# Kernel tuning notes

Hardware: AMD Instinct MI355X
Metric: run time of the kernel (lower is better)

Reference implementation:

```python
import jax, jax.numpy as jnp
import numpy as np

B, N, DIM, H, DH, PDIM, ED = 2, 384, 256, 4, 64, 128, 16
EPS = 1e-8


def _ln(x, g, b):
    m = x.mean(-1, keepdims=True)
    v = ((x - m) ** 2).mean(-1, keepdims=True)
    return (x - m) / jnp.sqrt(v + 1e-5) * g + b


def setup_inputs() -> dict:
    key = jax.random.key(0)
    ks = iter(jax.random.split(key, 48))
    def rn(shape, s=0.02):
        return jax.random.normal(next(ks), shape, jnp.float32) * s
    z = lambda *s: jnp.zeros(s, jnp.float32)
    o = lambda *s: jnp.ones(s, jnp.float32)
    return dict(
        feats=jax.random.normal(next(ks), (B, N, DIM), jnp.float32),
        coors=jax.random.normal(next(ks), (B, N, 3), jnp.float32),
        edges=jax.random.normal(next(ks), (B, N, N, ED), jnp.float32),
        gamma=o(DIM),
        w_qkv=rn((DIM, 3 * H * DH)),
        w_gate=z(DIM, 2 * H), b_gate=jnp.full((2 * H,), 10.0, jnp.float32),
        w_th=rn((H, H), 0.3),
        w_e1=rn((H + ED, 2 * (H + ED))), w_e2=rn((2 * (H + ED), H)),
        w_c=rn((H, H)),
        w_cg=rn((H, H)), b_cg=z(H),
        coors_scale=o(1),
        coors_combine=jax.random.normal(next(ks), (H,), jnp.float32),
        pb_w0=rn((1, PDIM)), pb_b0=z(PDIM), pb_g0=o(PDIM), pb_be0=z(PDIM),
        pb_w1=rn((PDIM, PDIM)), pb_b1=z(PDIM), pb_g1=o(PDIM), pb_be1=z(PDIM),
        pb_w2=rn((PDIM, PDIM)), pb_b2=z(PDIM), pb_g2=o(PDIM), pb_be2=z(PDIM),
        w_qkpos=rn((PDIM, H)), b_qkpos=z(H),
        w_vpos=rn((PDIM, H * DH)), b_vpos=z(H * DH),
        w_out=rn((H * DH, DIM)), b_out=z(DIM),
    )


def reference(feats, coors, edges, gamma, w_qkv, w_gate, b_gate, w_th, w_e1, w_e2,
              w_c, w_cg, b_cg, coors_scale, coors_combine,
              pb_w0, pb_b0, pb_g0, pb_be0, pb_w1, pb_b1, pb_g1, pb_be1,
              pb_w2, pb_b2, pb_g2, pb_be2, w_qkpos, b_qkpos, w_vpos, b_vpos,
              w_out, b_out):
    b, n, _ = feats.shape
    h, dh = H, DH
    x = _ln(feats, gamma, 0.0)                                  # pre-norm (beta is a zero buffer)
    rel_coors = coors[:, :, None, :] - coors[:, None, :, :]      # b i j 3
    rel_dist = jnp.linalg.norm(rel_coors, axis=-1)               # b i j

    qkv = x @ w_qkv
    q, k, v = jnp.split(qkv, 3, axis=-1)
    q = q.reshape(b, n, h, dh).transpose(0, 2, 1, 3)             # b h n d
    k = k.reshape(b, n, h, dh).transpose(0, 2, 1, 3)
    v = v.reshape(b, n, h, dh).transpose(0, 2, 1, 3)

    gates = jax.nn.sigmoid(x @ w_gate + b_gate).reshape(b, n, 2, h)
    out_gate = gates[:, :, 0].transpose(0, 2, 1)[..., None]      # b h n 1
    rel_out_gate = gates[:, :, 1].transpose(0, 2, 1)[..., None]  # b h n 1

    # dynamic position bias MLP on pairwise distances (input_dim=1)
    p = rel_dist[..., None]                                      # b i j 1
    p = jax.nn.silu(_ln(p @ pb_w0 + pb_b0, pb_g0, pb_be0))
    p = jax.nn.silu(_ln(p @ pb_w1 + pb_b1, pb_g1, pb_be1))
    p = jax.nn.silu(_ln(p @ pb_w2 + pb_b2, pb_g2, pb_be2))       # b i j pdim
    qk_pos = (p @ w_qkpos + b_qkpos).transpose(0, 3, 1, 2)       # b h i j
    value_pos = (p @ w_vpos + b_vpos).reshape(b, n, n, h, dh).transpose(0, 3, 1, 2, 4)  # b h i j d

    q = q * (dh ** -0.5)
    qk = jnp.einsum('bhid,bhjd->bhij', q, k) + qk_pos            # b h i j

    # edge MLP fused with per-head scores
    qk_e = jnp.concatenate([qk.transpose(0, 2, 3, 1), edges], axis=-1)  # b i j (h+ed)
    cmi = jax.nn.gelu(qk_e @ w_e1, approximate=False) @ w_e2     # b i j h
    qk = cmi.transpose(0, 3, 1, 2)                               # b h i j

    # coordinate attention branch (edge variant: GELU -> Linear(h,h))
    coor_weights = jax.nn.gelu(cmi, approximate=False) @ w_c     # b i j h
    coor_attn = jax.nn.softmax(coor_weights, axis=-2)            # softmax over j
    rel_sign = cmi @ w_cg + b_cg                                 # b i j h

    nrm = jnp.linalg.norm(rel_coors, axis=-1, keepdims=True)
    rel_norm = rel_coors / jnp.maximum(nrm, EPS) * coors_scale   # CoorsNorm, b i j 3

    attn = jax.nn.softmax(qk, axis=-1)
    attn = jnp.einsum('hg,bgij->bhij', w_th, attn)               # talking heads 1x1 conv

    node_out = jnp.einsum('bhij,bhjd->bhid', attn, v) \
             + jnp.einsum('bhij,bhijd->bhid', attn, value_pos)   # b h i d

    w = coor_attn * rel_sign                                     # b i j h
    coors_out = jnp.einsum('bijh,bijc->bhic', w, rel_norm)       # b h i 3

    node_out = node_out * out_gate
    coors_out = coors_out * rel_out_gate
    coors_out = jnp.einsum('bhic,h->bic', coors_out, coors_combine)
    node_out = node_out.transpose(0, 2, 1, 3).reshape(b, n, h * dh)
    return node_out @ w_out + b_out, coors_out
```

## Files before the change

kernel.cpp:

```cpp
#include <hip/hip_runtime.h>
#include <hip/hip_bf16.h>

#define B_   2
#define N_   384
#define DIM_ 256
#define H_   4
#define DH_  64
#define PD_  128
#define ED_  16
#define NU2_ ((B_ * N_ * N_) / 16)

typedef _Float16 v8h __attribute__((ext_vector_type(8)));
typedef float    v4f __attribute__((ext_vector_type(4)));

__device__ __forceinline__ float rcp_(float x) { return __builtin_amdgcn_rcpf(x); }

__device__ __forceinline__ float erf_fast(float x) {
    float ax = fabsf(x);
    float t = rcp_(fmaf(0.3275911f, ax, 1.0f));
    float y = t * fmaf(t, fmaf(t, fmaf(t, fmaf(t, 1.061405429f, -1.453152027f),
                                       1.421413741f), -0.284496736f), 0.254829592f);
    float r = 1.0f - y * __expf(-ax * ax);
    return (x < 0.f) ? -r : r;
}
__device__ __forceinline__ float gelu_(float x) {
    return 0.5f * x * (1.0f + erf_fast(x * 0.70710678118654752f));
}
__device__ __forceinline__ float silu_(float x) {
    return x * rcp_(1.0f + __expf(-x));
}

__device__ __forceinline__ float4 block_reduce256_f4(float4 v, float4* red) {
    #pragma unroll
    for (int o = 32; o > 0; o >>= 1) {
        v.x += __shfl_xor(v.x, o); v.y += __shfl_xor(v.y, o);
        v.z += __shfl_xor(v.z, o); v.w += __shfl_xor(v.w, o);
    }
    __syncthreads();
    if ((threadIdx.x & 63) == 0) red[threadIdx.x >> 6] = v;
    __syncthreads();
    float4 r = red[0];
    #pragma unroll
    for (int w2 = 1; w2 < 4; w2++) {
        float4 o = red[w2];
        r.x += o.x; r.y += o.y; r.z += o.z; r.w += o.w;
    }
    return r;
}

__device__ __forceinline__ float4 block_reduce4(float4 v, bool ismax, float4* red, int slot) {
    #pragma unroll
    for (int o = 32; o > 0; o >>= 1) {
        float x = __shfl_xor(v.x, o), y = __shfl_xor(v.y, o);
        float z = __shfl_xor(v.z, o), w = __shfl_xor(v.w, o);
        if (ismax) { v.x = fmaxf(v.x, x); v.y = fmaxf(v.y, y); v.z = fmaxf(v.z, z); v.w = fmaxf(v.w, w); }
        else       { v.x += x; v.y += y; v.z += z; v.w += w; }
    }
    if ((threadIdx.x & 63) == 0) red[slot * 8 + (threadIdx.x >> 6)] = v;
    __syncthreads();
    float4 r = red[slot * 8];
    #pragma unroll
    for (int w2 = 1; w2 < 6; w2++) {
        float4 o = red[slot * 8 + w2];
        if (ismax) { r.x = fmaxf(r.x, o.x); r.y = fmaxf(r.y, o.y); r.z = fmaxf(r.z, o.z); r.w = fmaxf(r.w, o.w); }
        else       { r.x += o.x; r.y += o.y; r.z += o.z; r.w += o.w; }
    }
    return r;
}

__global__ __launch_bounds__(256) void eq_k1(
    const float* __restrict__ feats, const float* __restrict__ gamma,
    const float* __restrict__ w_qkv, const float* __restrict__ w_gate,
    const float* __restrict__ b_gate,
    _Float16* __restrict__ qh, _Float16* __restrict__ kh, float* __restrict__ v,
    float* __restrict__ og, float* __restrict__ rg) {
    const int r0 = blockIdx.x * 4;
    const int b = r0 / N_;
    const int t = threadIdx.x;
    __shared__ float xs[4][DIM_];
    __shared__ float4 red4k[4];
    float4 f;
    f.x = feats[(long)(r0 + 0) * DIM_ + t];
    f.y = feats[(long)(r0 + 1) * DIM_ + t];
    f.z = feats[(long)(r0 + 2) * DIM_ + t];
    f.w = feats[(long)(r0 + 3) * DIM_ + t];
    float4 s = block_reduce256_f4(f, red4k);
    float4 mean = make_float4(s.x * (1.f/DIM_), s.y * (1.f/DIM_), s.z * (1.f/DIM_), s.w * (1.f/DIM_));
    float4 d = make_float4(f.x - mean.x, f.y - mean.y, f.z - mean.z, f.w - mean.w);
    float4 vr = block_reduce256_f4(make_float4(d.x*d.x, d.y*d.y, d.z*d.z, d.w*d.w), red4k);
    float g = gamma[t];
    xs[0][t] = d.x * rsqrtf(vr.x * (1.f/DIM_) + 1e-5f) * g;
    xs[1][t] = d.y * rsqrtf(vr.y * (1.f/DIM_) + 1e-5f) * g;
    xs[2][t] = d.z * rsqrtf(vr.z * (1.f/DIM_) + 1e-5f) * g;
    xs[3][t] = d.w * rsqrtf(vr.w * (1.f/DIM_) + 1e-5f) * g;
    __syncthreads();
    float acc[12];
    #pragma unroll
    for (int k = 0; k < 12; k++) acc[k] = 0.f;
    for (int c = 0; c < DIM_; c++) {
        const float* wr = w_qkv + (long)c * 768;
        float w0 = wr[t], w1 = wr[t + 256], w2 = wr[t + 512];
        #pragma unroll
        for (int r = 0; r < 4; r++) {
            float xc = xs[r][c];
            acc[r * 3 + 0] += xc * w0;
            acc[r * 3 + 1] += xc * w1;
            acc[r * 3 + 2] += xc * w2;
        }
    }
    int h = t >> 6, dd = t & 63;
    #pragma unroll
    for (int r = 0; r < 4; r++) {
        int n = r0 + r - b * N_;
        long idx = ((long)(b * H_ + h) * N_ + n) * DH_ + dd;
        qh[idx] = (_Float16)(acc[r * 3 + 0] * 0.125f);
        kh[idx] = (_Float16)(acc[r * 3 + 1]);
        v[idx]  = acc[r * 3 + 2];
    }
    if (t < 32) {
        int rr = t >> 3, gg = t & 7;
        float a = b_gate[gg];
        for (int c = 0; c < DIM_; c++) a += xs[rr][c] * w_gate[c * 8 + gg];
        float gv = rcp_(1.0f + __expf(-a));
        int n = r0 + rr - b * N_;
        if (gg < 4) og[(b * H_ + gg) * N_ + n] = gv;
        else        rg[(b * H_ + (gg - 4)) * N_ + n] = gv;
    }
}

#define MFMA16(a, b, c) __builtin_amdgcn_mfma_f32_16x16x32_f16(a, b, c, 0, 0, 0)

#define LNAPPLY(gr_, ber_)                                                        \
{                                                                                  \
    _Pragma("unroll")                                                              \
    for (int rg2 = 0; rg2 < 4; rg2++) {                                            \
        float s = 0.f, sq = 0.f;                                                   \
        _Pragma("unroll")                                                          \
        for (int nt = 0; nt < 8; nt++) {                                           \
            float v0 = acc[nt][rg2]; s += v0; sq += v0 * v0;                       \
        }                                                                          \
        s += __shfl_xor(s, 1); sq += __shfl_xor(sq, 1);                            \
        s += __shfl_xor(s, 2); sq += __shfl_xor(sq, 2);                            \
        s += __shfl_xor(s, 4); sq += __shfl_xor(sq, 4);                            \
        s += __shfl_xor(s, 8); sq += __shfl_xor(sq, 8);                            \
        float mean = s * (1.f / 128.f);                                            \
        float inv = rsqrtf(sq * (1.f / 128.f) - mean * mean + 1e-5f);              \
        int row2 = quad * 4 + rg2;                                                 \
        _Pragma("unroll")                                                          \
        for (int nt = 0; nt < 8; nt++) {                                           \
            float y = (acc[nt][rg2] - mean) * inv * gr_[nt] + ber_[nt];            \
            myslice[row2 * 136 + nt * 16 + l15] = (_Float16)silu_(y);              \
        }                                                                          \
    }                                                                              \
}

__global__ __launch_bounds__(512) __attribute__((amdgpu_waves_per_eu(2, 2)))
void eq_k2(
    const float* __restrict__ coors,
    const float* __restrict__ w0, const float* __restrict__ b0,
    const float* __restrict__ g0, const float* __restrict__ be0,
    const float* __restrict__ W1g, const float* __restrict__ b1,
    const float* __restrict__ g1, const float* __restrict__ be1,
    const float* __restrict__ W2g, const float* __restrict__ b2,
    const float* __restrict__ g2, const float* __restrict__ be2,
    const float* __restrict__ wqk, const float* __restrict__ bqk,
    const _Float16* __restrict__ qh, const _Float16* __restrict__ kh,
    _Float16* __restrict__ pT, float* __restrict__ qkpos,
    float* __restrict__ qkq) {

    extern __shared__ char smem[];
    _Float16* W1T    = (_Float16*)smem;
    _Float16* W2T    = (_Float16*)(smem + 34816);
    _Float16* slices = (_Float16*)(smem + 69632);
    _Float16* wqT    = (_Float16*)(smem + 104448);
    float*    PQR    = (float*)(smem + 108800);

    const int t = threadIdx.x;
    const int lane = t & 63, wv = t >> 6;
    const int l15 = lane & 15, quad = lane >> 4;
    _Float16* myslice = slices + wv * (16 * 136);

    for (int idx = t; idx < 16384; idx += 512) {
        int k = idx >> 7, n = idx & 127;
        W1T[n * 136 + k] = (_Float16)W1g[idx];
        W2T[n * 136 + k] = (_Float16)W2g[idx];
    }
    for (int idx = t; idx < 2048; idx += 512) {
        int n = idx >> 7, k = idx & 127;
        wqT[n * 136 + k] = (n < 4) ? (_Float16)wqk[k * 4 + n] : (_Float16)0.f;
    }
    float Sw = 0, Sb = 0, Sww = 0, Swb = 0, Sbb = 0;
    for (int c = 0; c < 128; c++) {
        float w = w0[c], bb2v = b0[c];
        Sw += w; Sb += bb2v; Sww += w * w; Swb += w * bb2v; Sbb += bb2v * bb2v;
    }
    const float mw = Sw * (1.f / 128.f), mbb = Sb * (1.f / 128.f);
    const float A2 = Sww * (1.f / 128.f) - mw * mw;
    const float AD = Swb * (1.f / 128.f) - mw * mbb;
    const float D2 = Sbb * (1.f / 128.f) - mbb * mbb;
    if (t < 128) {
        PQR[t]       = (w0[t] - mw) * g0[t];
        PQR[128 + t] = (b0[t] - mbb) * g0[t];
        PQR[256 + t] = be0[t];
    }
    float b1r[8], b2r[8], g1r[8], be1r[8], g2r[8], be2r[8];
    #pragma unroll
    for (int nt = 0; nt < 8; nt++) {
        int c = nt * 16 + l15;
        b1r[nt] = b1[c]; b2r[nt] = b2[c];
        g1r[nt] = g1[c]; be1r[nt] = be1[c];
        g2r[nt] = g2[c]; be2r[nt] = be2[c];
    }
    const float bqv = (l15 < 4) ? bqk[l15] : 0.f;
    __syncthreads();

    for (int unit = blockIdx.x * 8 + wv; unit < NU2_; unit += 256 * 8) {
        const int P0w = unit * 16;
        const int b = P0w / (N_ * N_);
        const int rem = P0w - b * (N_ * N_);
        const int ii = rem / N_;
        const int j0 = rem - ii * N_;
        const long bi = (long)(b * N_ + ii);
        const float cix = coors[(b * N_ + ii) * 3 + 0];
        const float ciy = coors[(b * N_ + ii) * 3 + 1];
        const float ciz = coors[(b * N_ + ii) * 3 + 2];
        float tt, uu;
        {
            int j = j0 + l15;
            float dx = cix - coors[(b * N_ + j) * 3 + 0];
            float dy = ciy - coors[(b * N_ + j) * 3 + 1];
            float dz = ciz - coors[(b * N_ + j) * 3 + 2];
            float d = sqrtf(dx * dx + dy * dy + dz * dz);
            float var = (d * d) * A2 + 2.f * d * AD + D2;
            float inv = rsqrtf(var + 1e-5f);
            tt = d * inv; uu = inv;
        }
        v8h A[4];
        #pragma unroll
        for (int kt = 0; kt < 4; kt++) {
            int base = kt * 32 + quad * 8;
            float4 Pa = *(const float4*)&PQR[base],       Pb = *(const float4*)&PQR[base + 4];
            float4 Qa = *(const float4*)&PQR[128 + base], Qb = *(const float4*)&PQR[128 + base + 4];
            float4 Ra = *(const float4*)&PQR[256 + base], Rb = *(const float4*)&PQR[256 + base + 4];
            float Pj[8] = {Pa.x, Pa.y, Pa.z, Pa.w, Pb.x, Pb.y, Pb.z, Pb.w};
            float Qj[8] = {Qa.x, Qa.y, Qa.z, Qa.w, Qb.x, Qb.y, Qb.z, Qb.w};
            float Rj[8] = {Ra.x, Ra.y, Ra.z, Ra.w, Rb.x, Rb.y, Rb.z, Rb.w};
            v8h av;
            #pragma unroll
            for (int jj = 0; jj < 8; jj++) {
                float y = tt * Pj[jj] + uu * Qj[jj] + Rj[jj];
                av[jj] = (_Float16)silu_(y);
            }
            A[kt] = av;
        }
        v4f acc[8];
        #pragma unroll
        for (int nt = 0; nt < 8; nt++) {
            v4f ci = {b1r[nt], b1r[nt], b1r[nt], b1r[nt]};
            acc[nt] = ci;
        }
        #pragma unroll
        for (int kt = 0; kt < 4; kt++) {
            #pragma unroll
            for (int nt = 0; nt < 8; nt++) {
                v8h Bv = *(const v8h*)&W1T[(nt * 16 + l15) * 136 + kt * 32 + quad * 8];
                acc[nt] = MFMA16(A[kt], Bv, acc[nt]);
            }
        }
        LNAPPLY(g1r, be1r)
        #pragma unroll
        for (int kt = 0; kt < 4; kt++)
            A[kt] = *(const v8h*)&myslice[l15 * 136 + kt * 32 + quad * 8];
        #pragma unroll
        for (int nt = 0; nt < 8; nt++) {
            v4f ci = {b2r[nt], b2r[nt], b2r[nt], b2r[nt]};
            acc[nt] = ci;
        }
        #pragma unroll
        for (int kt = 0; kt < 4; kt++) {
            #pragma unroll
            for (int nt = 0; nt < 8; nt++) {
                v8h Bv = *(const v8h*)&W2T[(nt * 16 + l15) * 136 + kt * 32 + quad * 8];
                acc[nt] = MFMA16(A[kt], Bv, acc[nt]);
            }
        }
        LNAPPLY(g2r, be2r)
        {
            _Float16* chunk = pT + (((long)bi * 24 + (j0 >> 4)) << 11);
            #pragma unroll
            for (int cc = 0; cc < 2; cc++) {
                int c = lane + cc * 64;
                v8h lo, hi;
                #pragma unroll
                for (int k = 0; k < 8; k++) {
                    lo[k] = myslice[k * 136 + c];
                    hi[k] = myslice[(k + 8) * 136 + c];
                }
                *(v8h*)(chunk + c * 16)     = lo;
                *(v8h*)(chunk + c * 16 + 8) = hi;
            }
        }
        {
            v4f c = {0.f, 0.f, 0.f, 0.f};
            #pragma unroll
            for (int kt = 0; kt < 4; kt++) {
                v8h av = *(const v8h*)&myslice[l15 * 136 + kt * 32 + quad * 8];
                v8h wq = *(const v8h*)&wqT[l15 * 136 + kt * 32 + quad * 8];
                c = MFMA16(av, wq, c);
            }
            if (l15 < 4) {
                #pragma unroll
                for (int rg2 = 0; rg2 < 4; rg2++) {
                    int row = quad * 4 + rg2;
                    qkpos[(long)(P0w + row) * 4 + l15] = c[rg2] + bqv;
                }
            }
        }
    }

    {
        int gw = blockIdx.x * 8 + wv;
        if (gw < 384) {
            const int bh = gw / 48;
            const int rest = gw - bh * 48;
            const int it = rest >> 1, nh = rest & 1;
            const int bb = bh >> 2, hh = bh & 3;
            const int i0 = it * 16;
            v8h A0 = *(const v8h*)&qh[((long)(bh * N_) + i0 + l15) * DH_ + quad * 8];
            v8h A1 = *(const v8h*)&qh[((long)(bh * N_) + i0 + l15) * DH_ + 32 + quad * 8];
            #pragma unroll 1
            for (int nt = 0; nt < 12; nt++) {
                int jq0 = nh * 192 + nt * 16;
                v8h B0 = *(const v8h*)&kh[((long)(bh * N_) + jq0 + l15) * DH_ + quad * 8];
                v8h B1 = *(const v8h*)&kh[((long)(bh * N_) + jq0 + l15) * DH_ + 32 + quad * 8];
                v4f c = {0.f, 0.f, 0.f, 0.f};
                c = MFMA16(A0, B0, c);
                c = MFMA16(A1, B1, c);
                #pragma unroll
                for (int rg2 = 0; rg2 < 4; rg2++) {
                    int i = i0 + quad * 4 + rg2;
                    int j = jq0 + l15;
                    long idx = (((long)(bb * N_ + i)) * N_ + j) * 4 + hh;
                    qkq[idx] = c[rg2];
                }
            }
        }
    }
}

__global__ __launch_bounds__(384) void eq_k3m(
    const float* __restrict__ edges, const float* __restrict__ qkpos,
    const float* __restrict__ qkq,
    const _Float16* __restrict__ pT, const float* __restrict__ v,
    const float* __restrict__ coors,
    const float* __restrict__ w_e1, const float* __restrict__ w_e2,
    const float* __restrict__ w_c, const float* __restrict__ w_cg,
    const float* __restrict__ b_cg, const float* __restrict__ w_th,
    const float* __restrict__ cscale, const float* __restrict__ ccomb,
    const float* __restrict__ og, const float* __restrict__ rg,
    const float* __restrict__ w_vpos, const float* __restrict__ b_vpos,
    const float* __restrict__ w_out, const float* __restrict__ b_out,
    float* __restrict__ out0, float* __restrict__ out1) {
    int row = blockIdx.x;
    int b = row / N_, i = row - b * N_;
    int j = threadIdx.x;
    __shared__ float we1[20 * 40];
    __shared__ float we2[40 * 4];
    __shared__ float wcs[16], wcgs[16], bcgs[4], wths[16];
    __shared__ float attnS[4 * N_];
    __shared__ float apS[2 * 4 * PD_];
    __shared__ float nodeS[256];
    __shared__ float4 red4[34];

    for (int idx = j; idx < 800; idx += 384) we1[idx] = w_e1[idx];
    if (j < 160) we2[j] = w_e2[j];
    if (j < 16) { wcs[j] = w_c[j]; wcgs[j] = w_cg[j]; wths[j] = w_th[j]; }
    if (j < 4) bcgs[j] = b_cg[j];
    __syncthreads();

    long pair = ((long)row) * N_ + j;
    float in20[20];
    {
        float4 qp = *(const float4*)(qkpos + pair * 4);
        float4 qq = *(const float4*)(qkq + pair * 4);
        in20[0] = qp.x + qq.x; in20[1] = qp.y + qq.y;
        in20[2] = qp.z + qq.z; in20[3] = qp.w + qq.w;
    }
    const float4* ep = (const float4*)(edges + pair * ED_);
    float4 e0 = ep[0], e1 = ep[1], e2 = ep[2], e3 = ep[3];
    in20[4] = e0.x;  in20[5] = e0.y;  in20[6] = e0.z;  in20[7] = e0.w;
    in20[8] = e1.x;  in20[9] = e1.y;  in20[10] = e1.z; in20[11] = e1.w;
    in20[12] = e2.x; in20[13] = e2.y; in20[14] = e2.z; in20[15] = e2.w;
    in20[16] = e3.x; in20[17] = e3.y; in20[18] = e3.z; in20[19] = e3.w;

    float c0 = 0, c1 = 0, c2 = 0, c3 = 0;
    #pragma unroll 1
    for (int oc = 0; oc < 5; oc++) {
        float a8[8] = {0.f, 0.f, 0.f, 0.f, 0.f, 0.f, 0.f, 0.f};
        #pragma unroll
        for (int c = 0; c < 20; c++) {
            float xc = in20[c];
            float4 wa = *(const float4*)&we1[c * 40 + oc * 8];
            float4 wb = *(const float4*)&we1[c * 40 + oc * 8 + 4];
            a8[0] += xc * wa.x; a8[1] += xc * wa.y; a8[2] += xc * wa.z; a8[3] += xc * wa.w;
            a8[4] += xc * wb.x; a8[5] += xc * wb.y; a8[6] += xc * wb.z; a8[7] += xc * wb.w;
        }
        #pragma unroll
        for (int o = 0; o < 8; o++) {
            float gg = gelu_(a8[o]);
            float4 w2v = *(const float4*)&we2[(oc * 8 + o) * 4];
            c0 += gg * w2v.x; c1 += gg * w2v.y; c2 += gg * w2v.z; c3 += gg * w2v.w;
        }
    }
    float cmi[4] = {c0, c1, c2, c3};
    float gc[4], cp[4], rs[4];
    #pragma unroll
    for (int h = 0; h < 4; h++) gc[h] = gelu_(cmi[h]);
    #pragma unroll
    for (int h = 0; h < 4; h++) {
        cp[h] = gc[0] * wcs[h] + gc[1] * wcs[4 + h] + gc[2] * wcs[8 + h] + gc[3] * wcs[12 + h];
        rs[h] = cmi[0] * wcgs[h] + cmi[1] * wcgs[4 + h] + cmi[2] * wcgs[8 + h] + cmi[3] * wcgs[12 + h] + bcgs[h];
    }

    float4 m4 = block_reduce4(make_float4(cmi[0], cmi[1], cmi[2], cmi[3]), true, red4, 0);
    float e[4];
    e[0] = __expf(cmi[0] - m4.x); e[1] = __expf(cmi[1] - m4.y);
    e[2] = __expf(cmi[2] - m4.z); e[3] = __expf(cmi[3] - m4.w);
    float4 l4 = block_reduce4(make_float4(e[0], e[1], e[2], e[3]), false, red4, 1);
    float sm[4] = {e[0] * rcp_(l4.x), e[1] * rcp_(l4.y), e[2] * rcp_(l4.z), e[3] * rcp_(l4.w)};
    #pragma unroll
    for (int h = 0; h < 4; h++)
        attnS[h * N_ + j] = wths[h * 4 + 0] * sm[0] + wths[h * 4 + 1] * sm[1]
                          + wths[h * 4 + 2] * sm[2] + wths[h * 4 + 3] * sm[3];

    float dx = coors[(b * N_ + i) * 3 + 0] - coors[(b * N_ + j) * 3 + 0];
    float dy = coors[(b * N_ + i) * 3 + 1] - coors[(b * N_ + j) * 3 + 1];
    float dz = coors[(b * N_ + i) * 3 + 2] - coors[(b * N_ + j) * 3 + 2];
    float nrm = sqrtf(dx * dx + dy * dy + dz * dz);
    float sc = cscale[0] * rcp_(fmaxf(nrm, 1e-8f));
    float rx = dx * sc, ry = dy * sc, rz = dz * sc;
    float4 cm4 = block_reduce4(make_float4(cp[0], cp[1], cp[2], cp[3]), true, red4, 0);
    float ec[4];
    ec[0] = __expf(cp[0] - cm4.x); ec[1] = __expf(cp[1] - cm4.y);
    ec[2] = __expf(cp[2] - cm4.z); ec[3] = __expf(cp[3] - cm4.w);
    float4 cl4 = block_reduce4(make_float4(ec[0], ec[1], ec[2], ec[3]), false, red4, 1);
    float w[4] = {ec[0] * rcp_(cl4.x) * rs[0], ec[1] * rcp_(cl4.y) * rs[1],
                  ec[2] * rcp_(cl4.z) * rs[2], ec[3] * rcp_(cl4.w) * rs[3]};
    float rv[12];
    #pragma unroll
    for (int h = 0; h < 4; h++) { rv[h] = w[h] * rx; rv[4 + h] = w[h] * ry; rv[8 + h] = w[h] * rz; }
    #pragma unroll
    for (int o = 32; o > 0; o >>= 1) {
        #pragma unroll
        for (int k = 0; k < 12; k++) rv[k] += __shfl_xor(rv[k], o);
    }
    if ((j & 63) == 0) {
        int wid = j >> 6;
        red4[16 + wid * 3 + 0] = make_float4(rv[0], rv[1], rv[2], rv[3]);
        red4[16 + wid * 3 + 1] = make_float4(rv[4], rv[5], rv[6], rv[7]);
        red4[16 + wid * 3 + 2] = make_float4(rv[8], rv[9], rv[10], rv[11]);
    }
    __syncthreads();
    if (j == 0) {
        float4 sx4 = red4[16], sy4 = red4[17], sz4 = red4[18];
        #pragma unroll
        for (int w2 = 1; w2 < 6; w2++) {
            float4 ax = red4[16 + w2 * 3 + 0], ay = red4[16 + w2 * 3 + 1], az = red4[16 + w2 * 3 + 2];
            sx4.x += ax.x; sx4.y += ax.y; sx4.z += ax.z; sx4.w += ax.w;
            sy4.x += ay.x; sy4.y += ay.y; sy4.z += ay.z; sy4.w += ay.w;
            sz4.x += az.x; sz4.y += az.y; sz4.z += az.z; sz4.w += az.w;
        }
        float f0 = ccomb[0] * rg[(b * H_ + 0) * N_ + i];
        float f1 = ccomb[1] * rg[(b * H_ + 1) * N_ + i];
        float f2 = ccomb[2] * rg[(b * H_ + 2) * N_ + i];
        float f3 = ccomb[3] * rg[(b * H_ + 3) * N_ + i];
        out1[(b * N_ + i) * 3 + 0] = f0 * sx4.x + f1 * sx4.y + f2 * sx4.z + f3 * sx4.w;
        out1[(b * N_ + i) * 3 + 1] = f0 * sy4.x + f1 * sy4.y + f2 * sy4.z + f3 * sy4.w;
        out1[(b * N_ + i) * 3 + 2] = f0 * sz4.x + f1 * sz4.y + f2 * sz4.z + f3 * sz4.w;
    }

    if (j < 128) {
        const int lane = j & 63, l15d = lane & 15, quadd = lane >> 4;
        const int parity = j >> 6;
        const int hh = l15d & 3;
        const float msk = (l15d < 4) ? 1.f : 0.f;
        v4f acc[8];
        #pragma unroll
        for (int nt = 0; nt < 8; nt++) { v4f z = {0.f, 0.f, 0.f, 0.f}; acc[nt] = z; }
        #pragma unroll 2
        for (int kth = 0; kth < 6; kth++) {
            int kt = parity * 6 + kth;
            float4 a0 = *(const float4*)&attnS[hh * N_ + kt * 32 + quadd * 8];
            float4 a1 = *(const float4*)&attnS[hh * N_ + kt * 32 + quadd * 8 + 4];
            v8h Af;
            Af[0] = (_Float16)(a0.x * msk); Af[1] = (_Float16)(a0.y * msk);
            Af[2] = (_Float16)(a0.z * msk); Af[3] = (_Float16)(a0.w * msk);
            Af[4] = (_Float16)(a1.x * msk); Af[5] = (_Float16)(a1.y * msk);
            Af[6] = (_Float16)(a1.z * msk); Af[7] = (_Float16)(a1.w * msk);
            const _Float16* chunkp = pT + (((long)row * 24 + kt * 2 + (quadd >> 1)) << 11)
                                        + ((quadd & 1) << 3);
            #pragma unroll
            for (int nt = 0; nt < 8; nt++) {
                v8h Bv = *(const v8h*)&chunkp[(nt * 16 + l15d) * 16];
                acc[nt] = MFMA16(Af, Bv, acc[nt]);
            }
        }
        if (quadd == 0) {
            #pragma unroll
            for (int nt = 0; nt < 8; nt++)
                #pragma unroll
                for (int rg2 = 0; rg2 < 4; rg2++)
                    apS[parity * 512 + rg2 * 128 + nt * 16 + l15d] = acc[nt][rg2];
        }
    } else {
        int tt = j - 128, h = tt >> 6, d = tt & 63;
        float acc = 0;
        const float* vp = v + ((long)(b * H_ + h) * N_) * DH_ + d;
        #pragma unroll 16
        for (int jj = 0; jj < N_; jj++) acc += attnS[h * N_ + jj] * vp[(long)jj * DH_];
        nodeS[tt] = acc;
    }
    __syncthreads();

    float nv = 0;
    if (j < 256) {
        int h = j >> 6, d = j & 63;
        float accp = 0;
        const float* wv = w_vpos + h * DH_ + d;
        #pragma unroll 8
        for (int c = 0; c < PD_; c++)
            accp += (apS[h * 128 + c] + apS[512 + h * 128 + c]) * wv[(long)c * (H_ * DH_)];
        float Sh = wths[h * 4 + 0] + wths[h * 4 + 1] + wths[h * 4 + 2] + wths[h * 4 + 3];
        nv = (nodeS[j] + accp + Sh * b_vpos[h * DH_ + d]) * og[(b * H_ + h) * N_ + i];
    }
    __syncthreads();
    if (j < 256) nodeS[j] = nv;
    __syncthreads();

    if (j < 256) {
        float acc = b_out[j];
        const float* wo = w_out + j;
        #pragma unroll 4
        for (int c4 = 0; c4 < 64; c4++) {
            float4 nv4 = *(const float4*)&nodeS[c4 * 4];
            acc += nv4.x * wo[(long)(c4 * 4 + 0) * 256]
                 + nv4.y * wo[(long)(c4 * 4 + 1) * 256]
                 + nv4.z * wo[(long)(c4 * 4 + 2) * 256]
                 + nv4.w * wo[(long)(c4 * 4 + 3) * 256];
        }
        out0[(long)row * 256 + j] = acc;
    }
}

extern "C" void kernel_launch(void* const* d_in, const int* in_sizes, int n_in,
                              void* d_out, int out_size, void* d_ws, size_t ws_size,
                              hipStream_t stream) {
    (void)in_sizes; (void)n_in; (void)out_size; (void)ws_size;
    const float* feats   = (const float*)d_in[0];
    const float* coors   = (const float*)d_in[1];
    const float* edges   = (const float*)d_in[2];
    const float* gamma   = (const float*)d_in[3];
    const float* w_qkv   = (const float*)d_in[4];
    const float* w_gate  = (const float*)d_in[5];
    const float* b_gate  = (const float*)d_in[6];
    const float* w_th    = (const float*)d_in[7];
    const float* w_e1    = (const float*)d_in[8];
    const float* w_e2    = (const float*)d_in[9];
    const float* w_c     = (const float*)d_in[10];
    const float* w_cg    = (const float*)d_in[11];
    const float* b_cg    = (const float*)d_in[12];
    const float* cscale  = (const float*)d_in[13];
    const float* ccomb   = (const float*)d_in[14];
    const float* pb_w0   = (const float*)d_in[15];
    const float* pb_b0   = (const float*)d_in[16];
    const float* pb_g0   = (const float*)d_in[17];
    const float* pb_be0  = (const float*)d_in[18];
    const float* pb_w1   = (const float*)d_in[19];
    const float* pb_b1   = (const float*)d_in[20];
    const float* pb_g1   = (const float*)d_in[21];
    const float* pb_be1  = (const float*)d_in[22];
    const float* pb_w2   = (const float*)d_in[23];
    const float* pb_b2   = (const float*)d_in[24];
    const float* pb_g2   = (const float*)d_in[25];
    const float* pb_be2  = (const float*)d_in[26];
    const float* w_qkpos = (const float*)d_in[27];
    const float* b_qkpos = (const float*)d_in[28];
    const float* w_vpos  = (const float*)d_in[29];
    const float* b_vpos  = (const float*)d_in[30];
    const float* w_out   = (const float*)d_in[31];
    const float* b_out   = (const float*)d_in[32];

    char* ws = (char*)d_ws;
    _Float16* qh   = (_Float16*)(ws + 0);
    _Float16* kh   = (_Float16*)(ws + 393216);
    float* v       = (float*)(ws + 786432);
    float* og      = (float*)(ws + 1572864);
    float* rg      = (float*)(ws + 1585152);
    float* qkpos   = (float*)(ws + 1597440);
    _Float16* pT   = (_Float16*)(ws + 6316032);
    float* qkq     = (float*)(ws + 81813504);

    float* out0 = (float*)d_out;
    float* out1 = out0 + (long)B_ * N_ * DIM_;

    const int K2_LDS = 110336;
    hipFuncSetAttribute((const void*)eq_k2, hipFuncAttributeMaxDynamicSharedMemorySize, K2_LDS);

    eq_k1<<<192, 256, 0, stream>>>(feats, gamma, w_qkv, w_gate, b_gate, qh, kh, v, og, rg);
    eq_k2<<<256, 512, K2_LDS, stream>>>(coors, pb_w0, pb_b0, pb_g0, pb_be0,
                                        pb_w1, pb_b1, pb_g1, pb_be1,
                                        pb_w2, pb_b2, pb_g2, pb_be2,
                                        w_qkpos, b_qkpos, qh, kh, pT, qkpos, qkq);
    eq_k3m<<<B_ * N_, 384, 0, stream>>>(edges, qkpos, qkq, pT, v, coors,
                                        w_e1, w_e2, w_c, w_cg, b_cg, w_th,
                                        cscale, ccomb, og, rg,
                                        w_vpos, b_vpos, w_out, b_out, out0, out1);
}
```

Baseline: 338.1 us.

## Halve rows per block in QKV kernel, merge softmax reductions, vectorize LDS reads

The QKV/LayerNorm kernel now handles 2 rows per block instead of 4, doubling the grid to 384 blocks, and its gate projection is split across all threads with a shared-memory reduction instead of running on 32 threads. In the per-row attention kernel, the two softmax max/sum reductions are merged into paired 8-wide reductions, cutting the number of block barriers. The edge MLP weights are stored as fp16 in LDS, and the attention-times-V and value-position loops use float4 LDS reads with several accumulators. This adds more blocks, which means more redundant weight reads, and the fp16 weights carry a small precision risk.

```diff
diff --git a/kernel.cpp b/kernel.cpp
--- a/kernel.cpp
+++ b/kernel.cpp
@@ -30,42 +30,56 @@
     return x * rcp_(1.0f + __expf(-x));
 }
 
-__device__ __forceinline__ float4 block_reduce256_f4(float4 v, float4* red) {
+__device__ __forceinline__ float2 block_reduce256_f2(float2 v, float2* red) {
     #pragma unroll
     for (int o = 32; o > 0; o >>= 1) {
         v.x += __shfl_xor(v.x, o); v.y += __shfl_xor(v.y, o);
-        v.z += __shfl_xor(v.z, o); v.w += __shfl_xor(v.w, o);
     }
     __syncthreads();
     if ((threadIdx.x & 63) == 0) red[threadIdx.x >> 6] = v;
     __syncthreads();
-    float4 r = red[0];
+    float2 r = red[0];
     #pragma unroll
     for (int w2 = 1; w2 < 4; w2++) {
-        float4 o = red[w2];
-        r.x += o.x; r.y += o.y; r.z += o.z; r.w += o.w;
+        float2 o = red[w2];
+        r.x += o.x; r.y += o.y;
     }
     return r;
 }
 
-__device__ __forceinline__ float4 block_reduce4(float4 v, bool ismax, float4* red, int slot) {
+__device__ __forceinline__ void block_reduce8(float4& va, float4& vb, bool ismax,
+                                              float4* red, int base) {
     #pragma unroll
     for (int o = 32; o > 0; o >>= 1) {
-        float x = __shfl_xor(v.x, o), y = __shfl_xor(v.y, o);
-        float z = __shfl_xor(v.z, o), w = __shfl_xor(v.w, o);
-        if (ismax) { v.x = fmaxf(v.x, x); v.y = fmaxf(v.y, y); v.z = fmaxf(v.z, z); v.w = fmaxf(v.w, w); }
-        else       { v.x += x; v.y += y; v.z += z; v.w += w; }
-    }
-    if ((threadIdx.x & 63) == 0) red[slot * 8 + (threadIdx.x >> 6)] = v;
-    __syncthreads();
-    float4 r = red[slot * 8];
+        float ax = __shfl_xor(va.x, o), ay = __shfl_xor(va.y, o);
+        float az = __shfl_xor(va.z, o), aw = __shfl_xor(va.w, o);
+        float bx = __shfl_xor(vb.x, o), by = __shfl_xor(vb.y, o);
+        float bz = __shfl_xor(vb.z, o), bw = __shfl_xor(vb.w, o);
+        if (ismax) {
+            va.x = fmaxf(va.x, ax); va.y = fmaxf(va.y, ay); va.z = fmaxf(va.z, az); va.w = fmaxf(va.w, aw);
+            vb.x = fmaxf(vb.x, bx); vb.y = fmaxf(vb.y, by); vb.z = fmaxf(vb.z, bz); vb.w = fmaxf(vb.w, bw);
+        } else {
+            va.x += ax; va.y += ay; va.z += az; va.w += aw;
+            vb.x += bx; vb.y += by; vb.z += bz; vb.w += bw;
+        }
+    }
+    if ((threadIdx.x & 63) == 0) {
+        red[base * 8 + (threadIdx.x >> 6)]       = va;
+        red[(base + 1) * 8 + (threadIdx.x >> 6)] = vb;
+    }
+    __syncthreads();
+    va = red[base * 8]; vb = red[(base + 1) * 8];
     #pragma unroll
     for (int w2 = 1; w2 < 6; w2++) {
-        float4 o = red[slot * 8 + w2];
-        if (ismax) { r.x = fmaxf(r.x, o.x); r.y = fmaxf(r.y, o.y); r.z = fmaxf(r.z, o.z); r.w = fmaxf(r.w, o.w); }
-        else       { r.x += o.x; r.y += o.y; r.z += o.z; r.w += o.w; }
-    }
-    return r;
+        float4 oa = red[base * 8 + w2], ob = red[(base + 1) * 8 + w2];
+        if (ismax) {
+            va.x = fmaxf(va.x, oa.x); va.y = fmaxf(va.y, oa.y); va.z = fmaxf(va.z, oa.z); va.w = fmaxf(va.w, oa.w);
+            vb.x = fmaxf(vb.x, ob.x); vb.y = fmaxf(vb.y, ob.y); vb.z = fmaxf(vb.z, ob.z); vb.w = fmaxf(vb.w, ob.w);
+        } else {
+            va.x += oa.x; va.y += oa.y; va.z += oa.z; va.w += oa.w;
+            vb.x += ob.x; vb.y += ob.y; vb.z += ob.z; vb.w += ob.w;
+        }
+    }
 }
 
 __global__ __launch_bounds__(256) void eq_k1(
@@ -74,34 +88,31 @@
     const float* __restrict__ b_gate,
     _Float16* __restrict__ qh, _Float16* __restrict__ kh, float* __restrict__ v,
     float* __restrict__ og, float* __restrict__ rg) {
-    const int r0 = blockIdx.x * 4;
+    const int r0 = blockIdx.x * 2;
     const int b = r0 / N_;
     const int t = threadIdx.x;
-    __shared__ float xs[4][DIM_];
-    __shared__ float4 red4k[4];
-    float4 f;
+    __shared__ float xs[2][DIM_];
+    __shared__ float2 red2k[4];
+    __shared__ float gredS[16][17];
+    float2 f;
     f.x = feats[(long)(r0 + 0) * DIM_ + t];
     f.y = feats[(long)(r0 + 1) * DIM_ + t];
-    f.z = feats[(long)(r0 + 2) * DIM_ + t];
-    f.w = feats[(long)(r0 + 3) * DIM_ + t];
-    float4 s = block_reduce256_f4(f, red4k);
-    float4 mean = make_float4(s.x * (1.f/DIM_), s.y * (1.f/DIM_), s.z * (1.f/DIM_), s.w * (1.f/DIM_));
-    float4 d = make_float4(f.x - mean.x, f.y - mean.y, f.z - mean.z, f.w - mean.w);
-    float4 vr = block_reduce256_f4(make_float4(d.x*d.x, d.y*d.y, d.z*d.z, d.w*d.w), red4k);
+    float2 s = block_reduce256_f2(f, red2k);
+    float mx = s.x * (1.f/DIM_), my = s.y * (1.f/DIM_);
+    float2 d = make_float2(f.x - mx, f.y - my);
+    float2 vr = block_reduce256_f2(make_float2(d.x*d.x, d.y*d.y), red2k);
     float g = gamma[t];
     xs[0][t] = d.x * rsqrtf(vr.x * (1.f/DIM_) + 1e-5f) * g;
     xs[1][t] = d.y * rsqrtf(vr.y * (1.f/DIM_) + 1e-5f) * g;
-    xs[2][t] = d.z * rsqrtf(vr.z * (1.f/DIM_) + 1e-5f) * g;
-    xs[3][t] = d.w * rsqrtf(vr.w * (1.f/DIM_) + 1e-5f) * g;
-    __syncthreads();
-    float acc[12];
-    #pragma unroll
-    for (int k = 0; k < 12; k++) acc[k] = 0.f;
+    __syncthreads();
+    float acc[6];
+    #pragma unroll
+    for (int k = 0; k < 6; k++) acc[k] = 0.f;
     for (int c = 0; c < DIM_; c++) {
         const float* wr = w_qkv + (long)c * 768;
         float w0 = wr[t], w1 = wr[t + 256], w2 = wr[t + 512];
         #pragma unroll
-        for (int r = 0; r < 4; r++) {
+        for (int r = 0; r < 2; r++) {
             float xc = xs[r][c];
             acc[r * 3 + 0] += xc * w0;
             acc[r * 3 + 1] += xc * w1;
@@ -110,21 +121,34 @@
     }
     int h = t >> 6, dd = t & 63;
     #pragma unroll
-    for (int r = 0; r < 4; r++) {
+    for (int r = 0; r < 2; r++) {
         int n = r0 + r - b * N_;
         long idx = ((long)(b * H_ + h) * N_ + n) * DH_ + dd;
         qh[idx] = (_Float16)(acc[r * 3 + 0] * 0.125f);
         kh[idx] = (_Float16)(acc[r * 3 + 1]);
         v[idx]  = acc[r * 3 + 2];
     }
-    if (t < 32) {
-        int rr = t >> 3, gg = t & 7;
-        float a = b_gate[gg];
-        for (int c = 0; c < DIM_; c++) a += xs[rr][c] * w_gate[c * 8 + gg];
+    {
+        const int o = t & 15, chunk = t >> 4;
+        const int gg = o & 7, rr = o >> 3;
+        float part = 0.f;
+        #pragma unroll
+        for (int k = 0; k < 16; k++) {
+            int c = chunk * 16 + k;
+            part += xs[rr][c] * w_gate[c * 8 + gg];
+        }
+        gredS[chunk][o] = part;
+    }
+    __syncthreads();
+    if (t < 16) {
+        float a = b_gate[t & 7];
+        #pragma unroll
+        for (int k = 0; k < 16; k++) a += gredS[k][t];
         float gv = rcp_(1.0f + __expf(-a));
-        int n = r0 + rr - b * N_;
-        if (gg < 4) og[(b * H_ + gg) * N_ + n] = gv;
-        else        rg[(b * H_ + (gg - 4)) * N_ + n] = gv;
+        int rr2 = t >> 3, g2 = t & 7;
+        int n = r0 + rr2 - b * N_;
+        if (g2 < 4) og[(b * H_ + g2) * N_ + n] = gv;
+        else        rg[(b * H_ + (g2 - 4)) * N_ + n] = gv;
     }
 }
 
@@ -364,15 +388,15 @@
     int row = blockIdx.x;
     int b = row / N_, i = row - b * N_;
     int j = threadIdx.x;
-    __shared__ float we1[20 * 40];
+    __shared__ _Float16 we1h[20 * 40];
     __shared__ float we2[40 * 4];
     __shared__ float wcs[16], wcgs[16], bcgs[4], wths[16];
     __shared__ float attnS[4 * N_];
     __shared__ float apS[2 * 4 * PD_];
     __shared__ float nodeS[256];
-    __shared__ float4 red4[34];
-
-    for (int idx = j; idx < 800; idx += 384) we1[idx] = w_e1[idx];
+    __shared__ float4 red4[50];
+
+    for (int idx = j; idx < 800; idx += 384) we1h[idx] = (_Float16)w_e1[idx];
     if (j < 160) we2[j] = w_e2[j];
     if (j < 16) { wcs[j] = w_c[j]; wcgs[j] = w_cg[j]; wths[j] = w_th[j]; }
     if (j < 4) bcgs[j] = b_cg[j];
@@ -400,10 +424,9 @@
         #pragma unroll
         for (int c = 0; c < 20; c++) {
             float xc = in20[c];
-            float4 wa = *(const float4*)&we1[c * 40 + oc * 8];
-            float4 wb = *(const float4*)&we1[c * 40 + oc * 8 + 4];
-            a8[0] += xc * wa.x; a8[1] += xc * wa.y; a8[2] += xc * wa.z; a8[3] += xc * wa.w;
-            a8[4] += xc * wb.x; a8[5] += xc * wb.y; a8[6] += xc * wb.z; a8[7] += xc * wb.w;
+            v8h wv = *(const v8h*)&we1h[c * 40 + oc * 8];
+            #pragma unroll
+            for (int o2 = 0; o2 < 8; o2++) a8[o2] += xc * (float)wv[o2];
         }
         #pragma unroll
         for (int o = 0; o < 8; o++) {
@@ -421,17 +444,6 @@
         cp[h] = gc[0] * wcs[h] + gc[1] * wcs[4 + h] + gc[2] * wcs[8 + h] + gc[3] * wcs[12 + h];
         rs[h] = cmi[0] * wcgs[h] + cmi[1] * wcgs[4 + h] + cmi[2] * wcgs[8 + h] + cmi[3] * wcgs[12 + h] + bcgs[h];
     }
-
-    float4 m4 = block_reduce4(make_float4(cmi[0], cmi[1], cmi[2], cmi[3]), true, red4, 0);
-    float e[4];
-    e[0] = __expf(cmi[0] - m4.x); e[1] = __expf(cmi[1] - m4.y);
-    e[2] = __expf(cmi[2] - m4.z); e[3] = __expf(cmi[3] - m4.w);
-    float4 l4 = block_reduce4(make_float4(e[0], e[1], e[2], e[3]), false, red4, 1);
-    float sm[4] = {e[0] * rcp_(l4.x), e[1] * rcp_(l4.y), e[2] * rcp_(l4.z), e[3] * rcp_(l4.w)};
-    #pragma unroll
-    for (int h = 0; h < 4; h++)
-        attnS[h * N_ + j] = wths[h * 4 + 0] * sm[0] + wths[h * 4 + 1] * sm[1]
-                          + wths[h * 4 + 2] * sm[2] + wths[h * 4 + 3] * sm[3];
 
     float dx = coors[(b * N_ + i) * 3 + 0] - coors[(b * N_ + j) * 3 + 0];
     float dy = coors[(b * N_ + i) * 3 + 1] - coors[(b * N_ + j) * 3 + 1];
@@ -439,11 +451,25 @@
     float nrm = sqrtf(dx * dx + dy * dy + dz * dz);
     float sc = cscale[0] * rcp_(fmaxf(nrm, 1e-8f));
     float rx = dx * sc, ry = dy * sc, rz = dz * sc;
-    float4 cm4 = block_reduce4(make_float4(cp[0], cp[1], cp[2], cp[3]), true, red4, 0);
-    float ec[4];
+
+    float4 m4  = make_float4(cmi[0], cmi[1], cmi[2], cmi[3]);
+    float4 cm4 = make_float4(cp[0], cp[1], cp[2], cp[3]);
+    block_reduce8(m4, cm4, true, red4, 0);
+    float e[4], ec[4];
+    e[0] = __expf(cmi[0] - m4.x); e[1] = __expf(cmi[1] - m4.y);
+    e[2] = __expf(cmi[2] - m4.z); e[3] = __expf(cmi[3] - m4.w);
     ec[0] = __expf(cp[0] - cm4.x); ec[1] = __expf(cp[1] - cm4.y);
     ec[2] = __expf(cp[2] - cm4.z); ec[3] = __expf(cp[3] - cm4.w);
-    float4 cl4 = block_reduce4(make_float4(ec[0], ec[1], ec[2], ec[3]), false, red4, 1);
+    float4 l4  = make_float4(e[0], e[1], e[2], e[3]);
+    float4 cl4 = make_float4(ec[0], ec[1], ec[2], ec[3]);
+    block_reduce8(l4, cl4, false, red4, 2);
+
+    float sm[4] = {e[0] * rcp_(l4.x), e[1] * rcp_(l4.y), e[2] * rcp_(l4.z), e[3] * rcp_(l4.w)};
+    #pragma unroll
+    for (int h = 0; h < 4; h++)
+        attnS[h * N_ + j] = wths[h * 4 + 0] * sm[0] + wths[h * 4 + 1] * sm[1]
+                          + wths[h * 4 + 2] * sm[2] + wths[h * 4 + 3] * sm[3];
+
     float w[4] = {ec[0] * rcp_(cl4.x) * rs[0], ec[1] * rcp_(cl4.y) * rs[1],
                   ec[2] * rcp_(cl4.z) * rs[2], ec[3] * rcp_(cl4.w) * rs[3]};
     float rv[12];
@@ -456,16 +482,16 @@
     }
     if ((j & 63) == 0) {
         int wid = j >> 6;
-        red4[16 + wid * 3 + 0] = make_float4(rv[0], rv[1], rv[2], rv[3]);
-        red4[16 + wid * 3 + 1] = make_float4(rv[4], rv[5], rv[6], rv[7]);
-        red4[16 + wid * 3 + 2] = make_float4(rv[8], rv[9], rv[10], rv[11]);
+        red4[32 + wid * 3 + 0] = make_float4(rv[0], rv[1], rv[2], rv[3]);
+        red4[32 + wid * 3 + 1] = make_float4(rv[4], rv[5], rv[6], rv[7]);
+        red4[32 + wid * 3 + 2] = make_float4(rv[8], rv[9], rv[10], rv[11]);
     }
     __syncthreads();
     if (j == 0) {
-        float4 sx4 = red4[16], sy4 = red4[17], sz4 = red4[18];
+        float4 sx4 = red4[32], sy4 = red4[33], sz4 = red4[34];
         #pragma unroll
         for (int w2 = 1; w2 < 6; w2++) {
-            float4 ax = red4[16 + w2 * 3 + 0], ay = red4[16 + w2 * 3 + 1], az = red4[16 + w2 * 3 + 2];
+            float4 ax = red4[32 + w2 * 3 + 0], ay = red4[32 + w2 * 3 + 1], az = red4[32 + w2 * 3 + 2];
             sx4.x += ax.x; sx4.y += ax.y; sx4.z += ax.z; sx4.w += ax.w;
             sy4.x += ay.x; sy4.y += ay.y; sy4.z += ay.z; sy4.w += ay.w;
             sz4.x += az.x; sz4.y += az.y; sz4.z += az.z; sz4.w += az.w;
@@ -514,11 +540,17 @@
         }
     } else {
         int tt = j - 128, h = tt >> 6, d = tt & 63;
-        float acc = 0;
+        float acc0 = 0, acc1 = 0, acc2 = 0, acc3 = 0;
         const float* vp = v + ((long)(b * H_ + h) * N_) * DH_ + d;
-        #pragma unroll 16
-        for (int jj = 0; jj < N_; jj++) acc += attnS[h * N_ + jj] * vp[(long)jj * DH_];
-        nodeS[tt] = acc;
+        #pragma unroll 8
+        for (int jj = 0; jj < N_; jj += 4) {
+            float4 a = *(const float4*)&attnS[h * N_ + jj];
+            acc0 += a.x * vp[(long)(jj + 0) * DH_];
+            acc1 += a.y * vp[(long)(jj + 1) * DH_];
+            acc2 += a.z * vp[(long)(jj + 2) * DH_];
+            acc3 += a.w * vp[(long)(jj + 3) * DH_];
+        }
+        nodeS[tt] = (acc0 + acc1) + (acc2 + acc3);
     }
     __syncthreads();
 
@@ -527,9 +559,15 @@
         int h = j >> 6, d = j & 63;
         float accp = 0;
         const float* wv = w_vpos + h * DH_ + d;
-        #pragma unroll 8
-        for (int c = 0; c < PD_; c++)
-            accp += (apS[h * 128 + c] + apS[512 + h * 128 + c]) * wv[(long)c * (H_ * DH_)];
+        #pragma unroll 4
+        for (int c4 = 0; c4 < 32; c4++) {
+            float4 p0 = *(const float4*)&apS[h * 128 + c4 * 4];
+            float4 p1 = *(const float4*)&apS[512 + h * 128 + c4 * 4];
+            accp += (p0.x + p1.x) * wv[(long)(c4 * 4 + 0) * (H_ * DH_)]
+                  + (p0.y + p1.y) * wv[(long)(c4 * 4 + 1) * (H_ * DH_)]
+                  + (p0.z + p1.z) * wv[(long)(c4 * 4 + 2) * (H_ * DH_)]
+                  + (p0.w + p1.w) * wv[(long)(c4 * 4 + 3) * (H_ * DH_)];
+        }
         float Sh = wths[h * 4 + 0] + wths[h * 4 + 1] + wths[h * 4 + 2] + wths[h * 4 + 3];
         nv = (nodeS[j] + accp + Sh * b_vpos[h * DH_ + d]) * og[(b * H_ + h) * N_ + i];
     }
@@ -606,7 +644,7 @@
     const int K2_LDS = 110336;
     hipFuncSetAttribute((const void*)eq_k2, hipFuncAttributeMaxDynamicSharedMemorySize, K2_LDS);
 
-    eq_k1<<<192, 256, 0, stream>>>(feats, gamma, w_qkv, w_gate, b_gate, qh, kh, v, og, rg);
+    eq_k1<<<384, 256, 0, stream>>>(feats, gamma, w_qkv, w_gate, b_gate, qh, kh, v, og, rg);
     eq_k2<<<256, 512, K2_LDS, stream>>>(coors, pb_w0, pb_b0, pb_g0, pb_be0,
                                         pb_w1, pb_b1, pb_g1, pb_be1,
                                         pb_w2, pb_b2, pb_g2, pb_be2,
```

Result: faster. 306.5 us (-9.4%).
